# Optimization experiments

Hardware: AMD Instinct MI355X
Metric: run time of the kernel (lower is better)

## Reference

```python
import math
import jax, jax.numpy as jnp
import numpy as np


def _alibi_slopes(n):
    def pow2_slopes(n):
        start = 2.0 ** (-(2.0 ** (-(math.log2(n) - 3))))
        return [start * (start ** i) for i in range(n)]
    if math.log2(n).is_integer():
        return pow2_slopes(n)
    cp2 = 2 ** math.floor(math.log2(n))
    return pow2_slopes(cp2) + _alibi_slopes(2 * cp2)[0::2][: n - cp2]


NUM_HEADS = 16


def setup_inputs() -> dict:
    key = jax.random.key(0)
    ks = jax.random.split(key, 5)
    B, S, H = 2, 2048, 2048
    return {
        "hidden_states": jax.random.normal(ks[0], (B, S, H), jnp.float32),
        "w_qkv": jax.random.normal(ks[1], (H, 3 * H), jnp.float32) * (H ** -0.5),
        "b_qkv": jax.random.normal(ks[2], (3 * H,), jnp.float32) * 0.02,
        "w_proj": jax.random.normal(ks[3], (H, H), jnp.float32) * (H ** -0.5),
        "b_proj": jax.random.normal(ks[4], (H,), jnp.float32) * 0.02,
    }


def reference(hidden_states, w_qkv, b_qkv, w_proj, b_proj):
    B, S, H = hidden_states.shape
    nh = NUM_HEADS
    hd = H // nh
    scale = 1.0 / hd  # mup scale_qk_dot_by_d=True -> d^-1 (not d^-0.5)

    qkv = hidden_states @ w_qkv + b_qkv  # [B,S,3H]
    q, k, v = jnp.split(qkv, 3, axis=-1)
    q = q.reshape(B, S, nh, hd)
    k = k.reshape(B, S, nh, hd)
    v = v.reshape(B, S, nh, hd)

    scores = jnp.einsum("bqhd,bkhd->bhqk", q, k) * scale  # [B,nh,S,S]

    slopes = jnp.asarray(_alibi_slopes(nh), dtype=scores.dtype)  # [nh]
    pos = jnp.arange(S)
    rel = (pos[None, :] - pos[:, None]).astype(scores.dtype)  # j - i, <=0 in causal region
    bias = slopes[:, None, None] * rel[None, :, :]  # [nh,S,S]
    causal = pos[None, :] <= pos[:, None]  # [S,S]

    scores = jnp.where(causal[None, None], scores + bias[None], jnp.finfo(scores.dtype).min)
    attn = jax.nn.softmax(scores, axis=-1)

    out = jnp.einsum("bhqk,bkhd->bqhd", attn, v).reshape(B, S, H)
    return out @ w_proj + b_proj
```

## Files before the change

kernel.cpp:

```cpp
#include <hip/hip_runtime.h>
#include <hip/hip_bf16.h>

typedef short bf16x8 __attribute__((ext_vector_type(8)));
typedef float f32x4 __attribute__((ext_vector_type(4)));
typedef unsigned short ushort_t;

#define NH 16
#define HD 128
#define SEQ 2048
#define HID 2048
#define NQKV 6144
#define BATCH 2

__device__ __forceinline__ ushort_t f2bf(float x) {
    unsigned u = __builtin_bit_cast(unsigned, x);
    u = (u + 0x7fffu + ((u >> 16) & 1u)) >> 16;
    return (ushort_t)u;
}

__device__ __forceinline__ void gl2lds16(const ushort_t* g, ushort_t* l) {
    __builtin_amdgcn_global_load_lds(
        (__attribute__((address_space(1))) void*)(g),
        (__attribute__((address_space(3))) void*)(l), 16, 0, 0);
}

__global__ __launch_bounds__(256) void prep_fused(
    const float* __restrict__ hidden, ushort_t* __restrict__ hbf,
    const float* __restrict__ wqkv, ushort_t* __restrict__ wqkvT,
    const float* __restrict__ wproj, ushort_t* __restrict__ wprojT) {
    const int bid = blockIdx.x;
    const int t = threadIdx.x;
    if (bid >= 12288 && bid < 16384) {
        int i = (bid - 12288) * 256 + t;
        float4 a0 = *(const float4*)(hidden + (size_t)i * 8);
        float4 a1 = *(const float4*)(hidden + (size_t)i * 8 + 4);
        union { ushort_t u[8]; uint4 v; } p;
        p.u[0]=f2bf(a0.x); p.u[1]=f2bf(a0.y); p.u[2]=f2bf(a0.z); p.u[3]=f2bf(a0.w);
        p.u[4]=f2bf(a1.x); p.u[5]=f2bf(a1.y); p.u[6]=f2bf(a1.z); p.u[7]=f2bf(a1.w);
        *(uint4*)(hbf + (size_t)i * 8) = p.v;
        return;
    }
    const float* w;
    ushort_t* wT;
    int N, bx, by;
    if (bid < 12288) {
        w = wqkv; wT = wqkvT; N = NQKV;
        bx = bid % 192; by = bid / 192;
    } else {
        int b2 = bid - 16384;
        w = wproj; wT = wprojT; N = HID;
        bx = b2 % 64; by = b2 / 64;
    }
    __shared__ float tile[32][33];
    const int nb = bx * 32, kb = by * 32;
    const int tx = t & 31, ty = t >> 5;
#pragma unroll
    for (int i = 0; i < 4; ++i) {
        int k = kb + ty + i * 8;
        tile[ty + i * 8][tx] = w[(size_t)k * N + nb + tx];
    }
    __syncthreads();
#pragma unroll
    for (int i = 0; i < 4; ++i) {
        int n = nb + ty + i * 8;
        wT[(size_t)n * HID + kb + tx] = f2bf(tile[tx][ty + i * 8]);
    }
}

#define GEMM_KLOOP(A_, BT_)                                                     \
    const int t = threadIdx.x;                                                  \
    const int w = t >> 6, lane = t & 63, lm = lane & 15, lq = lane >> 4;        \
    const int wm = (w >> 1) * 64, wn = (w & 1) * 64;                            \
    const int lrow = lane >> 3, lsw = (lane & 7) ^ lrow;                        \
    f32x4 acc[4][4] = {};                                                       \
    const ushort_t* gA = A_ + (size_t)(mb + w * 32 + lrow) * HID + lsw * 8;     \
    const ushort_t* gB = BT_ + (size_t)(nb + w * 32 + lrow) * HID + lsw * 8;    \
    for (int kb = 0; kb < HID; kb += 64) {                                      \
        __syncthreads();                                                        \
        _Pragma("unroll")                                                       \
        for (int c = 0; c < 4; ++c) {                                           \
            gl2lds16(gA + (size_t)c * 8 * HID + kb, At + (w * 256 + c * 64) * 8); \
            gl2lds16(gB + (size_t)c * 8 * HID + kb, Bt + (w * 256 + c * 64) * 8); \
        }                                                                       \
        __syncthreads();                                                        \
        _Pragma("unroll")                                                       \
        for (int kc = 0; kc < 2; ++kc) {                                        \
            const int slot = (kc * 4 + lq) ^ (lm & 7);                          \
            bf16x8 af[4], bfr[4];                                               \
            _Pragma("unroll")                                                   \
            for (int mt = 0; mt < 4; ++mt)                                      \
                af[mt] = ((const bf16x8*)At)[(wm + mt * 16 + lm) * 8 + slot];   \
            _Pragma("unroll")                                                   \
            for (int nt = 0; nt < 4; ++nt)                                      \
                bfr[nt] = ((const bf16x8*)Bt)[(wn + nt * 16 + lm) * 8 + slot];  \
            _Pragma("unroll")                                                   \
            for (int mt = 0; mt < 4; ++mt)                                      \
                _Pragma("unroll")                                               \
                for (int nt = 0; nt < 4; ++nt)                                  \
                    acc[mt][nt] = __builtin_amdgcn_mfma_f32_16x16x32_bf16(      \
                        af[mt], bfr[nt], acc[mt][nt], 0, 0, 0);                 \
        }                                                                       \
    }

__global__ __launch_bounds__(256) void gemm_qkv(
    const ushort_t* __restrict__ A, const ushort_t* __restrict__ BT,
    const float* __restrict__ bias,
    ushort_t* __restrict__ qbuf, ushort_t* __restrict__ kbuf,
    ushort_t* __restrict__ vTbuf) {
    __shared__ unsigned shbuf[128 * 68];
    ushort_t* At = (ushort_t*)shbuf;
    ushort_t* Bt = At + 128 * 64;
    const int mb = blockIdx.x * 128;
    const int nb = blockIdx.y * 128;
    GEMM_KLOOP(A, BT)

    const int sec = nb >> 11;
    if (sec < 2) {
#pragma unroll
        for (int mt = 0; mt < 4; ++mt)
#pragma unroll
            for (int nt = 0; nt < 4; ++nt)
#pragma unroll
                for (int r = 0; r < 4; ++r) {
                    int m = mb + wm + mt * 16 + lq * 4 + r;
                    int c = nb + wn + nt * 16 + lm;
                    float val = acc[mt][nt][r] + bias[c];
                    int h = (c >> 7) & 15;
                    int d = c & 127;
                    int b = m >> 11, s = m & 2047;
                    size_t bh = (size_t)(b * NH + h);
                    ushort_t* dst = (sec == 0) ? qbuf : kbuf;
                    dst[(bh * SEQ + s) * HD + d] = f2bf(val);
                }
    } else {
        __syncthreads();
        unsigned* T = shbuf;
#pragma unroll
        for (int mt = 0; mt < 4; ++mt)
#pragma unroll
            for (int nt = 0; nt < 4; ++nt) {
                const int cl = wn + nt * 16 + lm;
                const int ml = wm + mt * 16 + lq * 4;
                const float bb = bias[nb + cl];
#pragma unroll
                for (int r = 0; r < 4; r += 2) {
                    unsigned pk = (unsigned)f2bf(acc[mt][nt][r] + bb) |
                                  ((unsigned)f2bf(acc[mt][nt][r + 1] + bb) << 16);
                    T[cl * 68 + ((ml + r) >> 1)] = pk;
                }
            }
        __syncthreads();
        const int d = t & 127, sh = t >> 7;
        const int b = mb >> 11, sbase = mb & 2047;
        const int hv = (nb >> 7) - 32;
        ushort_t* vrow = vTbuf + ((size_t)(b * NH + hv) * HD + d) * SEQ + sbase + sh * 64;
#pragma unroll
        for (int i = 0; i < 8; ++i)
            *(uint4*)(vrow + i * 8) = *(const uint4*)&T[d * 68 + sh * 32 + i * 4];
    }
}

__global__ __launch_bounds__(256) void gemm_proj(
    const ushort_t* __restrict__ A, const ushort_t* __restrict__ BT,
    const float* __restrict__ bias, float* __restrict__ out) {
    __shared__ ushort_t Abuf[128 * 64];
    __shared__ ushort_t Bbuf[128 * 64];
    ushort_t* At = Abuf;
    ushort_t* Bt = Bbuf;
    const int mb = blockIdx.x * 128;
    const int nb = blockIdx.y * 128;
    GEMM_KLOOP(A, BT)
#pragma unroll
    for (int mt = 0; mt < 4; ++mt)
#pragma unroll
        for (int nt = 0; nt < 4; ++nt)
#pragma unroll
            for (int r = 0; r < 4; ++r) {
                int m = mb + wm + mt * 16 + lq * 4 + r;
                int c = nb + wn + nt * 16 + lm;
                out[(size_t)m * HID + c] = acc[mt][nt][r] + bias[c];
            }
}

__global__ __launch_bounds__(256) void attn_kernel(
    const ushort_t* __restrict__ qb, const ushort_t* __restrict__ kbuf,
    const ushort_t* __restrict__ vT, ushort_t* __restrict__ ob) {
    __shared__ ushort_t Ks[2][64 * 128];
    __shared__ ushort_t Vs[2][128 * 64];
    __shared__ ushort_t Ps[4][16 * 72];

    const int bid = blockIdx.x;
    const int x = bid & 7, g = bid >> 3;
    const int qt = 31 - (g >> 2);
    const int bh = ((g & 3) << 3) | x;
    const int qbase = qt * 64;
    const int t = threadIdx.x, w = t >> 6, lane = t & 63;
    const int lm = lane & 15, lq = lane >> 4;

    const ushort_t* Qg = qb + (size_t)bh * SEQ * HD;
    const ushort_t* Kg = kbuf + (size_t)bh * SEQ * HD;
    const ushort_t* Vg = vT + (size_t)bh * HD * SEQ;

    const float LOG2E = 1.44269504f;
    const int h = bh & 15;
    const float slope2 = exp2f(-0.5f * (float)(h + 1)) * LOG2E;
    const float scale2 = (1.0f / 128.0f) * LOG2E;

    const int qg = qbase + w * 16 + lm;

    bf16x8 qf[4];
#pragma unroll
    for (int kc = 0; kc < 4; ++kc) {
        uint4 qv = *(const uint4*)(Qg + (size_t)qg * HD + kc * 32 + lq * 8);
        qf[kc] = __builtin_bit_cast(bf16x8, qv);
    }

    float foff[4][4];
#pragma unroll
    for (int mt = 0; mt < 4; ++mt)
#pragma unroll
        for (int r = 0; r < 4; ++r)
            foff[mt][r] = slope2 * (float)(mt * 16 + lq * 4 + r);

    int koffs[4], voffs[4];
#pragma unroll
    for (int i = 0; i < 4; ++i) {
        int ci = i * 256 + t;
        int kr = ci >> 4, ks = ci & 15;
        int kcg = (ks & 8) | ((ks & 7) ^ (kr & 7));
        koffs[i] = kr * HD + kcg * 8;
        int vr = ci >> 3, vs = ci & 7;
        int vcg = vs ^ (vr & 7);
        voffs[i] = vr * SEQ + vcg * 8;
    }

#define ATTN_STAGE(KT, BUF)                                                   \
    {                                                                         \
        const ushort_t* Kt_ = Kg + (size_t)(KT) * 64 * HD;                    \
        const ushort_t* Vt_ = Vg + (size_t)(KT) * 64;                         \
        _Pragma("unroll")                                                     \
        for (int i = 0; i < 4; ++i) {                                         \
            gl2lds16(Kt_ + koffs[i], Ks[BUF] + (i * 256 + w * 64) * 8);       \
            gl2lds16(Vt_ + voffs[i], Vs[BUF] + (i * 256 + w * 64) * 8);       \
        }                                                                     \
    }

    float mrow = -1e30f, lrow = 0.0f;
    f32x4 O[8] = {};
    const int nkt = qt + 1;

    ATTN_STAGE(0, 0)
    __syncthreads();

    for (int kt = 0; kt < nkt; ++kt) {
        const int cur = kt & 1;
        if (kt + 1 < nkt) ATTN_STAGE(kt + 1, cur ^ 1)

        f32x4 sacc[4] = {};
        __builtin_amdgcn_s_setprio(1);
#pragma unroll
        for (int kc = 0; kc < 4; ++kc) {
            const int slot = ((kc * 4 + lq) & 8) | (((kc * 4 + lq) & 7) ^ (lm & 7));
#pragma unroll
            for (int mt = 0; mt < 4; ++mt) {
                bf16x8 bk = *(const bf16x8*)&Ks[cur][((mt * 16 + lm) * 16 + slot) * 8];
                sacc[mt] = __builtin_amdgcn_mfma_f32_16x16x32_bf16(bk, qf[kc], sacc[mt], 0, 0, 0);
            }
        }
        __builtin_amdgcn_s_setprio(0);

        const float sbase = slope2 * (float)(kt * 64 - qg);
        float sc[4][4];
        if (kt == qt) {
#pragma unroll
            for (int mt = 0; mt < 4; ++mt)
#pragma unroll
                for (int r = 0; r < 4; ++r) {
                    float s = sacc[mt][r] * scale2 + (sbase + foff[mt][r]);
                    sc[mt][r] = (kt * 64 + mt * 16 + lq * 4 + r <= qg) ? s : -3e38f;
                }
        } else {
#pragma unroll
            for (int mt = 0; mt < 4; ++mt)
#pragma unroll
                for (int r = 0; r < 4; ++r)
                    sc[mt][r] = sacc[mt][r] * scale2 + (sbase + foff[mt][r]);
        }

        float tm = sc[0][0];
#pragma unroll
        for (int mt = 0; mt < 4; ++mt)
#pragma unroll
            for (int r = 0; r < 4; ++r) tm = fmaxf(tm, sc[mt][r]);
        tm = fmaxf(tm, __shfl_xor(tm, 16));
        tm = fmaxf(tm, __shfl_xor(tm, 32));

        const bool noresc = __all(tm <= mrow + 8.0f) && (kt > 0);
        float mnew, alpha;
        if (noresc) {
            mnew = mrow;
            alpha = 1.0f;
        } else {
            mnew = fmaxf(mrow, tm);
            alpha = __builtin_amdgcn_exp2f(mrow - mnew);
        }
        mrow = mnew;

        float psum = 0.0f;
#pragma unroll
        for (int mt = 0; mt < 4; ++mt) {
            float p0 = __builtin_amdgcn_exp2f(sc[mt][0] - mnew);
            float p1 = __builtin_amdgcn_exp2f(sc[mt][1] - mnew);
            float p2 = __builtin_amdgcn_exp2f(sc[mt][2] - mnew);
            float p3 = __builtin_amdgcn_exp2f(sc[mt][3] - mnew);
            psum += (p0 + p1) + (p2 + p3);
            uint2 wv;
            wv.x = ((unsigned)f2bf(p1) << 16) | f2bf(p0);
            wv.y = ((unsigned)f2bf(p3) << 16) | f2bf(p2);
            *(uint2*)&Ps[w][lm * 72 + mt * 16 + lq * 4] = wv;
        }
        psum += __shfl_xor(psum, 16);
        psum += __shfl_xor(psum, 32);
        lrow = lrow * alpha + psum;

        if (!noresc) {
            float av[4];
#pragma unroll
            for (int r = 0; r < 4; ++r) av[r] = __shfl(alpha, lq * 4 + r);
#pragma unroll
            for (int nt = 0; nt < 8; ++nt)
#pragma unroll
                for (int r = 0; r < 4; ++r) O[nt][r] *= av[r];
        }

        asm volatile("s_waitcnt lgkmcnt(0)" ::: "memory");
        __builtin_amdgcn_s_setprio(1);
#pragma unroll
        for (int kc2 = 0; kc2 < 2; ++kc2) {
            bf16x8 ap = *(const bf16x8*)&Ps[w][lm * 72 + kc2 * 32 + lq * 8];
            const int slot = (kc2 * 4 + lq) ^ (lm & 7);
#pragma unroll
            for (int nt = 0; nt < 8; ++nt) {
                bf16x8 bv = *(const bf16x8*)&Vs[cur][((nt * 16 + lm) * 8 + slot) * 8];
                O[nt] = __builtin_amdgcn_mfma_f32_16x16x32_bf16(ap, bv, O[nt], 0, 0, 0);
            }
        }
        __builtin_amdgcn_s_setprio(0);

        __syncthreads();
    }

    float lb[4];
#pragma unroll
    for (int r = 0; r < 4; ++r)
        lb[r] = __builtin_amdgcn_rcpf(__shfl(lrow, lq * 4 + r));
    const int b = bh >> 4;
#pragma unroll
    for (int nt = 0; nt < 8; ++nt)
#pragma unroll
        for (int r = 0; r < 4; ++r) {
            int s = qbase + w * 16 + lq * 4 + r;
            int d = nt * 16 + lm;
            ob[((size_t)(b * SEQ + s)) * HID + h * HD + d] = f2bf(O[nt][r] * lb[r]);
        }
#undef ATTN_STAGE
}

extern "C" void kernel_launch(void* const* d_in, const int* in_sizes, int n_in,
                              void* d_out, int out_size, void* d_ws, size_t ws_size,
                              hipStream_t stream) {
    const float* hidden = (const float*)d_in[0];
    const float* w_qkv = (const float*)d_in[1];
    const float* b_qkv = (const float*)d_in[2];
    const float* w_proj = (const float*)d_in[3];
    const float* b_proj = (const float*)d_in[4];
    float* out = (float*)d_out;

    char* ws = (char*)d_ws;
    size_t off = 0;
    ushort_t* wqkvT = (ushort_t*)(ws + off); off += (size_t)NQKV * HID * 2;
    ushort_t* wprojT = (ushort_t*)(ws + off); off += (size_t)HID * HID * 2;
    ushort_t* hbf = (ushort_t*)(ws + off); off += (size_t)BATCH * SEQ * HID * 2;
    ushort_t* qw = (ushort_t*)(ws + off); off += (size_t)BATCH * NH * SEQ * HD * 2;
    ushort_t* kw = (ushort_t*)(ws + off); off += (size_t)BATCH * NH * SEQ * HD * 2;
    ushort_t* vTw = (ushort_t*)(ws + off); off += (size_t)BATCH * NH * SEQ * HD * 2;
    ushort_t* attnw = (ushort_t*)(ws + off); off += (size_t)BATCH * SEQ * HID * 2;

    prep_fused<<<dim3(20480), 256, 0, stream>>>(
        hidden, hbf, w_qkv, wqkvT, w_proj, wprojT);

    gemm_qkv<<<dim3(BATCH * SEQ / 128, NQKV / 128), 256, 0, stream>>>(
        hbf, wqkvT, b_qkv, qw, kw, vTw);

    attn_kernel<<<dim3(BATCH * NH * 32), 256, 0, stream>>>(qw, kw, vTw, attnw);

    gemm_proj<<<dim3(BATCH * SEQ / 128, HID / 128), 256, 0, stream>>>(
        attnw, wprojT, b_proj, out);
}
```

Measured before the change: 365.6 us.

## Rewrite attention with 32x32 MFMA, 128-row query tiles and register-resident P

```diff
diff --git a/kernel.cpp b/kernel.cpp
--- a/kernel.cpp
+++ b/kernel.cpp
@@ -3,6 +3,7 @@
 
 typedef short bf16x8 __attribute__((ext_vector_type(8)));
 typedef float f32x4 __attribute__((ext_vector_type(4)));
+typedef float f32x16 __attribute__((ext_vector_type(16)));
 typedef unsigned short ushort_t;
 
 #define NH 16
@@ -16,6 +17,12 @@
     unsigned u = __builtin_bit_cast(unsigned, x);
     u = (u + 0x7fffu + ((u >> 16) & 1u)) >> 16;
     return (ushort_t)u;
+}
+
+__device__ __forceinline__ unsigned cvtpk(float lo, float hi) {
+    unsigned r;
+    asm("v_cvt_pk_bf16_f32 %0, %1, %2" : "=v"(r) : "v"(lo), "v"(hi));
+    return r;
 }
 
 __device__ __forceinline__ void gl2lds16(const ushort_t* g, ushort_t* l) {
@@ -185,42 +192,35 @@
 __global__ __launch_bounds__(256) void attn_kernel(
     const ushort_t* __restrict__ qb, const ushort_t* __restrict__ kbuf,
     const ushort_t* __restrict__ vT, ushort_t* __restrict__ ob) {
-    __shared__ ushort_t Ks[2][64 * 128];
-    __shared__ ushort_t Vs[2][128 * 64];
-    __shared__ ushort_t Ps[4][16 * 72];
+    __shared__ ushort_t Ks[64 * 128];
+    __shared__ ushort_t Vs[128 * 64];
 
     const int bid = blockIdx.x;
     const int x = bid & 7, g = bid >> 3;
-    const int qt = 31 - (g >> 2);
+    const int qt = 15 - (g >> 2);
     const int bh = ((g & 3) << 3) | x;
-    const int qbase = qt * 64;
+    const int qbase = qt * 128;
     const int t = threadIdx.x, w = t >> 6, lane = t & 63;
-    const int lm = lane & 15, lq = lane >> 4;
+    const int l31 = lane & 31, hl = lane >> 5;
 
     const ushort_t* Qg = qb + (size_t)bh * SEQ * HD;
     const ushort_t* Kg = kbuf + (size_t)bh * SEQ * HD;
     const ushort_t* Vg = vT + (size_t)bh * HD * SEQ;
 
+    const int h = bh & 15;
     const float LOG2E = 1.44269504f;
-    const int h = bh & 15;
     const float slope2 = exp2f(-0.5f * (float)(h + 1)) * LOG2E;
     const float scale2 = (1.0f / 128.0f) * LOG2E;
 
-    const int qg = qbase + w * 16 + lm;
-
-    bf16x8 qf[4];
-#pragma unroll
-    for (int kc = 0; kc < 4; ++kc) {
-        uint4 qv = *(const uint4*)(Qg + (size_t)qg * HD + kc * 32 + lq * 8);
-        qf[kc] = __builtin_bit_cast(bf16x8, qv);
-    }
-
-    float foff[4][4];
-#pragma unroll
-    for (int mt = 0; mt < 4; ++mt)
-#pragma unroll
-        for (int r = 0; r < 4; ++r)
-            foff[mt][r] = slope2 * (float)(mt * 16 + lq * 4 + r);
+    const int qrow = qbase + w * 32 + l31;
+    const int ktd = (qbase + w * 32 + 31) >> 6;
+
+    bf16x8 qf[8];
+#pragma unroll
+    for (int s = 0; s < 8; ++s) {
+        uint4 qv = *(const uint4*)(Qg + (size_t)qrow * HD + (2 * s + hl) * 8);
+        qf[s] = __builtin_bit_cast(bf16x8, qv);
+    }
 
     int koffs[4], voffs[4];
 #pragma unroll
@@ -234,136 +234,137 @@
         voffs[i] = vr * SEQ + vcg * 8;
     }
 
-#define ATTN_STAGE(KT, BUF)                                                   \
-    {                                                                         \
-        const ushort_t* Kt_ = Kg + (size_t)(KT) * 64 * HD;                    \
-        const ushort_t* Vt_ = Vg + (size_t)(KT) * 64;                         \
-        _Pragma("unroll")                                                     \
-        for (int i = 0; i < 4; ++i) {                                         \
-            gl2lds16(Kt_ + koffs[i], Ks[BUF] + (i * 256 + w * 64) * 8);       \
-            gl2lds16(Vt_ + voffs[i], Vs[BUF] + (i * 256 + w * 64) * 8);       \
-        }                                                                     \
-    }
-
     float mrow = -1e30f, lrow = 0.0f;
-    f32x4 O[8] = {};
-    const int nkt = qt + 1;
-
-    ATTN_STAGE(0, 0)
-    __syncthreads();
+    f32x16 O[4] = {};
+    const int nkt = 2 * qt + 2;
 
     for (int kt = 0; kt < nkt; ++kt) {
-        const int cur = kt & 1;
-        if (kt + 1 < nkt) ATTN_STAGE(kt + 1, cur ^ 1)
-
-        f32x4 sacc[4] = {};
+        __syncthreads();
+        {
+            const ushort_t* Kt_ = Kg + (size_t)kt * 64 * HD;
+            const ushort_t* Vt_ = Vg + (size_t)kt * 64;
+#pragma unroll
+            for (int i = 0; i < 4; ++i) {
+                gl2lds16(Kt_ + koffs[i], Ks + (i * 256 + w * 64) * 8);
+                gl2lds16(Vt_ + voffs[i], Vs + (i * 256 + w * 64) * 8);
+            }
+        }
+        __syncthreads();
+
+        if (kt > ktd) continue;
+
+        f32x16 s0 = {}, s1 = {};
         __builtin_amdgcn_s_setprio(1);
 #pragma unroll
-        for (int kc = 0; kc < 4; ++kc) {
-            const int slot = ((kc * 4 + lq) & 8) | (((kc * 4 + lq) & 7) ^ (lm & 7));
-#pragma unroll
-            for (int mt = 0; mt < 4; ++mt) {
-                bf16x8 bk = *(const bf16x8*)&Ks[cur][((mt * 16 + lm) * 16 + slot) * 8];
-                sacc[mt] = __builtin_amdgcn_mfma_f32_16x16x32_bf16(bk, qf[kc], sacc[mt], 0, 0, 0);
-            }
+        for (int s = 0; s < 8; ++s) {
+            const int c = 2 * s + hl;
+            const int slot = (c & 8) | ((c & 7) ^ (l31 & 7));
+            bf16x8 k0 = *(const bf16x8*)&Ks[(l31 * 16 + slot) * 8];
+            bf16x8 k1 = *(const bf16x8*)&Ks[((32 + l31) * 16 + slot) * 8];
+            s0 = __builtin_amdgcn_mfma_f32_32x32x16_bf16(k0, qf[s], s0, 0, 0, 0);
+            s1 = __builtin_amdgcn_mfma_f32_32x32x16_bf16(k1, qf[s], s1, 0, 0, 0);
         }
         __builtin_amdgcn_s_setprio(0);
 
-        const float sbase = slope2 * (float)(kt * 64 - qg);
-        float sc[4][4];
-        if (kt == qt) {
-#pragma unroll
-            for (int mt = 0; mt < 4; ++mt)
-#pragma unroll
-                for (int r = 0; r < 4; ++r) {
-                    float s = sacc[mt][r] * scale2 + (sbase + foff[mt][r]);
-                    sc[mt][r] = (kt * 64 + mt * 16 + lq * 4 + r <= qg) ? s : -3e38f;
-                }
+        const float sb = slope2 * (float)(kt * 64 + 4 * hl - qrow);
+        float tm = -3e38f;
+        if (kt == ktd) {
+#pragma unroll
+            for (int r = 0; r < 16; ++r) {
+                const int Cr = (r & 3) + 8 * (r >> 2);
+                float v0 = s0[r] * scale2 + (sb + slope2 * (float)Cr);
+                float v1 = s1[r] * scale2 + (sb + slope2 * (float)(Cr + 32));
+                int k0i = kt * 64 + Cr + 4 * hl;
+                v0 = (k0i <= qrow) ? v0 : -3e38f;
+                v1 = (k0i + 32 <= qrow) ? v1 : -3e38f;
+                s0[r] = v0; s1[r] = v1;
+                tm = fmaxf(tm, fmaxf(v0, v1));
+            }
         } else {
 #pragma unroll
-            for (int mt = 0; mt < 4; ++mt)
-#pragma unroll
-                for (int r = 0; r < 4; ++r)
-                    sc[mt][r] = sacc[mt][r] * scale2 + (sbase + foff[mt][r]);
-        }
-
-        float tm = sc[0][0];
-#pragma unroll
-        for (int mt = 0; mt < 4; ++mt)
-#pragma unroll
-            for (int r = 0; r < 4; ++r) tm = fmaxf(tm, sc[mt][r]);
-        tm = fmaxf(tm, __shfl_xor(tm, 16));
+            for (int r = 0; r < 16; ++r) {
+                const int Cr = (r & 3) + 8 * (r >> 2);
+                float v0 = s0[r] * scale2 + (sb + slope2 * (float)Cr);
+                float v1 = s1[r] * scale2 + (sb + slope2 * (float)(Cr + 32));
+                s0[r] = v0; s1[r] = v1;
+                tm = fmaxf(tm, fmaxf(v0, v1));
+            }
+        }
         tm = fmaxf(tm, __shfl_xor(tm, 32));
 
         const bool noresc = __all(tm <= mrow + 8.0f) && (kt > 0);
         float mnew, alpha;
-        if (noresc) {
-            mnew = mrow;
-            alpha = 1.0f;
-        } else {
-            mnew = fmaxf(mrow, tm);
-            alpha = __builtin_amdgcn_exp2f(mrow - mnew);
-        }
+        if (noresc) { mnew = mrow; alpha = 1.0f; }
+        else { mnew = fmaxf(mrow, tm); alpha = __builtin_amdgcn_exp2f(mrow - mnew); }
         mrow = mnew;
 
         float psum = 0.0f;
 #pragma unroll
-        for (int mt = 0; mt < 4; ++mt) {
-            float p0 = __builtin_amdgcn_exp2f(sc[mt][0] - mnew);
-            float p1 = __builtin_amdgcn_exp2f(sc[mt][1] - mnew);
-            float p2 = __builtin_amdgcn_exp2f(sc[mt][2] - mnew);
-            float p3 = __builtin_amdgcn_exp2f(sc[mt][3] - mnew);
-            psum += (p0 + p1) + (p2 + p3);
-            uint2 wv;
-            wv.x = ((unsigned)f2bf(p1) << 16) | f2bf(p0);
-            wv.y = ((unsigned)f2bf(p3) << 16) | f2bf(p2);
-            *(uint2*)&Ps[w][lm * 72 + mt * 16 + lq * 4] = wv;
-        }
-        psum += __shfl_xor(psum, 16);
+        for (int r = 0; r < 16; ++r) {
+            float p0 = __builtin_amdgcn_exp2f(s0[r] - mnew);
+            float p1 = __builtin_amdgcn_exp2f(s1[r] - mnew);
+            s0[r] = p0; s1[r] = p1;
+            psum += p0 + p1;
+        }
         psum += __shfl_xor(psum, 32);
         lrow = lrow * alpha + psum;
 
         if (!noresc) {
-            float av[4];
-#pragma unroll
-            for (int r = 0; r < 4; ++r) av[r] = __shfl(alpha, lq * 4 + r);
-#pragma unroll
-            for (int nt = 0; nt < 8; ++nt)
-#pragma unroll
-                for (int r = 0; r < 4; ++r) O[nt][r] *= av[r];
-        }
-
-        asm volatile("s_waitcnt lgkmcnt(0)" ::: "memory");
+#pragma unroll
+            for (int dt = 0; dt < 4; ++dt)
+#pragma unroll
+                for (int r = 0; r < 16; ++r) O[dt][r] *= alpha;
+        }
+
+        unsigned c0[8], c1[8];
+#pragma unroll
+        for (int G = 0; G < 4; ++G) {
+            c0[G]     = cvtpk(s0[4 * G + 0], s0[4 * G + 1]);
+            c1[G]     = cvtpk(s0[4 * G + 2], s0[4 * G + 3]);
+            c0[4 + G] = cvtpk(s1[4 * G + 0], s1[4 * G + 1]);
+            c1[4 + G] = cvtpk(s1[4 * G + 2], s1[4 * G + 3]);
+        }
+
         __builtin_amdgcn_s_setprio(1);
 #pragma unroll
-        for (int kc2 = 0; kc2 < 2; ++kc2) {
-            bf16x8 ap = *(const bf16x8*)&Ps[w][lm * 72 + kc2 * 32 + lq * 8];
-            const int slot = (kc2 * 4 + lq) ^ (lm & 7);
-#pragma unroll
-            for (int nt = 0; nt < 8; ++nt) {
-                bf16x8 bv = *(const bf16x8*)&Vs[cur][((nt * 16 + lm) * 8 + slot) * 8];
-                O[nt] = __builtin_amdgcn_mfma_f32_16x16x32_bf16(ap, bv, O[nt], 0, 0, 0);
+        for (int ks = 0; ks < 4; ++ks) {
+            unsigned a0 = c0[2 * ks], a1 = c1[2 * ks];
+            unsigned b0 = c0[2 * ks + 1], b1 = c1[2 * ks + 1];
+            unsigned own0 = hl ? b0 : a0, own1 = hl ? b1 : a1;
+            unsigned snd0 = hl ? a0 : b0, snd1 = hl ? a1 : b1;
+            unsigned rcv0 = __shfl_xor(snd0, 32);
+            unsigned rcv1 = __shfl_xor(snd1, 32);
+            union { unsigned u[4]; bf16x8 v; } pf;
+            pf.u[0] = hl ? rcv0 : own0;
+            pf.u[1] = hl ? rcv1 : own1;
+            pf.u[2] = hl ? own0 : rcv0;
+            pf.u[3] = hl ? own1 : rcv1;
+            const int c = 2 * ks + hl;
+#pragma unroll
+            for (int dt = 0; dt < 4; ++dt) {
+                const int vr = dt * 32 + l31;
+                const int slot = c ^ (vr & 7);
+                bf16x8 vf = *(const bf16x8*)&Vs[(vr * 8 + slot) * 8];
+                O[dt] = __builtin_amdgcn_mfma_f32_32x32x16_bf16(vf, pf.v, O[dt], 0, 0, 0);
             }
         }
         __builtin_amdgcn_s_setprio(0);
-
-        __syncthreads();
-    }
-
-    float lb[4];
-#pragma unroll
-    for (int r = 0; r < 4; ++r)
-        lb[r] = __builtin_amdgcn_rcpf(__shfl(lrow, lq * 4 + r));
+    }
+
+    const float lb = __builtin_amdgcn_rcpf(lrow);
     const int b = bh >> 4;
-#pragma unroll
-    for (int nt = 0; nt < 8; ++nt)
-#pragma unroll
-        for (int r = 0; r < 4; ++r) {
-            int s = qbase + w * 16 + lq * 4 + r;
-            int d = nt * 16 + lm;
-            ob[((size_t)(b * SEQ + s)) * HID + h * HD + d] = f2bf(O[nt][r] * lb[r]);
-        }
-#undef ATTN_STAGE
+    ushort_t* orow = ob + ((size_t)(b * SEQ + qrow)) * HID + h * HD;
+#pragma unroll
+    for (int dt = 0; dt < 4; ++dt)
+#pragma unroll
+        for (int g4 = 0; g4 < 4; ++g4) {
+            union { ushort_t u[4]; uint2 v; } pk;
+            pk.u[0] = f2bf(O[dt][4 * g4 + 0] * lb);
+            pk.u[1] = f2bf(O[dt][4 * g4 + 1] * lb);
+            pk.u[2] = f2bf(O[dt][4 * g4 + 2] * lb);
+            pk.u[3] = f2bf(O[dt][4 * g4 + 3] * lb);
+            *(uint2*)(orow + dt * 32 + 8 * g4 + 4 * hl) = pk.v;
+        }
 }
 
 extern "C" void kernel_launch(void* const* d_in, const int* in_sizes, int n_in,
@@ -392,7 +393,7 @@
     gemm_qkv<<<dim3(BATCH * SEQ / 128, NQKV / 128), 256, 0, stream>>>(
         hbf, wqkvT, b_qkv, qw, kw, vTw);
 
-    attn_kernel<<<dim3(BATCH * NH * 32), 256, 0, stream>>>(qw, kw, vTw, attnw);
+    attn_kernel<<<dim3(BATCH * NH * 16), 256, 0, stream>>>(qw, kw, vTw, attnw);
 
     gemm_proj<<<dim3(BATCH * SEQ / 128, HID / 128), 256, 0, stream>>>(
         attnw, wprojT, b_proj, out);
```

Measured after the change: 368.6 us (median of 2 runs). About the same (+0.8%).
